# Optimization experiments

Measured on AMD Instinct MI355X. Metric: run time of the kernel, lower is better.

## Reference

```python
import jax, jax.numpy as jnp
import numpy as np

H, DM, DK, DV, DFF = 8, 512, 64, 64, 2048
B, S = 8, 1024
EPS = 1e-5


def layernorm_global(x):
    # torch nn.LayerNorm(x.size()[1:], elementwise_affine=False): normalize over ALL dims except batch
    mu = jnp.mean(x, axis=(1, 2), keepdims=True)
    var = jnp.var(x, axis=(1, 2), keepdims=True)
    return (x - mu) / jnp.sqrt(var + EPS)


def mha(q_in, k_in, v_in, wq, bq, wk, bk, wv, bv, wo, bo, causal):
    # wq/wk: [h, dk, dmodel], wv: [h, dv, dmodel] (torch Linear weight layout [out,in])
    q = jnp.einsum('bsd,hkd->bhsk', q_in, wq) + bq[None, :, None, :]
    k = jnp.einsum('bsd,hkd->bhsk', k_in, wk) + bk[None, :, None, :]
    v = jnp.einsum('bsd,hvd->bhsv', v_in, wv) + bv[None, :, None, :]
    scores = jnp.einsum('bhqk,bhsk->bhqs', q, k) / np.sqrt(DK).astype(np.float32)
    if causal:
        Sq = q_in.shape[1]
        mask = jnp.triu(jnp.full((Sq, Sq), -jnp.inf, dtype=scores.dtype), k=1)
        scores = scores + mask[None, None, :, :]
    w = jax.nn.softmax(scores, axis=-1)
    attn = jnp.einsum('bhqs,bhsv->bhqv', w, v)  # [b,h,q,dv]
    concat = attn.transpose(0, 2, 1, 3).reshape(q_in.shape[0], q_in.shape[1], H * DV)
    return concat @ wo.T + bo


def setup_inputs() -> dict:
    key = jax.random.key(0)
    ks = jax.random.split(key, 24)
    f = lambda k, shape: (jax.random.normal(k, shape, dtype=jnp.float32) * 0.02)
    inp = {
        'x_enc': jax.random.normal(ks[0], (B, S, DM), dtype=jnp.float32),
        'x_dec': jax.random.normal(ks[1], (B, S, DM), dtype=jnp.float32),
        # masked self-attention params
        'mq_w': f(ks[2], (H, DK, DM)), 'mq_b': f(ks[3], (H, DK)),
        'mk_w': f(ks[4], (H, DK, DM)), 'mk_b': f(ks[5], (H, DK)),
        'mv_w': f(ks[6], (H, DV, DM)), 'mv_b': f(ks[7], (H, DV)),
        'mo_w': f(ks[8], (DM, H * DV)), 'mo_b': f(ks[9], (DM,)),
        # cross-attention params
        'cq_w': f(ks[10], (H, DK, DM)), 'cq_b': f(ks[11], (H, DK)),
        'ck_w': f(ks[12], (H, DK, DM)), 'ck_b': f(ks[13], (H, DK)),
        'cv_w': f(ks[14], (H, DV, DM)), 'cv_b': f(ks[15], (H, DV)),
        'co_w': f(ks[16], (DM, H * DV)), 'co_b': f(ks[17], (DM,)),
        # feedforward params
        'f1_w': f(ks[18], (DFF, DM)), 'f1_b': f(ks[19], (DFF,)),
        'f2_w': f(ks[20], (DM, DFF)), 'f2_b': f(ks[21], (DM,)),
    }
    return inp


def reference(x_enc, x_dec,
              mq_w, mq_b, mk_w, mk_b, mv_w, mv_b, mo_w, mo_b,
              cq_w, cq_b, ck_w, ck_b, cv_w, cv_b, co_w, co_b,
              f1_w, f1_b, f2_w, f2_b):
    # masked self-attention block (dropout = identity at eval)
    x_dec_n = layernorm_global(x_dec)
    sa = mha(x_dec_n, x_dec_n, x_dec_n, mq_w, mq_b, mk_w, mk_b, mv_w, mv_b, mo_w, mo_b, causal=True)
    current = x_dec + sa
    # cross-attention block
    cur_n = layernorm_global(current)
    enc_n = layernorm_global(x_enc)
    ca = mha(cur_n, enc_n, enc_n, cq_w, cq_b, ck_w, ck_b, cv_w, cv_b, co_w, co_b, causal=False)
    result = current + ca
    # feedforward block
    res_n = layernorm_global(result)
    ff = jax.nn.relu(res_n @ f1_w.T + f1_b) @ f2_w.T + f2_b
    return result + ff
```

## Files before the change

### kernel.cpp

```cpp
#include <hip/hip_runtime.h>
#include <cmath>
#include <cstddef>
#include <cstdint>

#define BN   8
#define SN   1024
#define DMN  512
#define HN   8
#define DKN  64
#define DFFN 2048

typedef short           bf16x8   __attribute__((ext_vector_type(8)));
typedef float           f32x4    __attribute__((ext_vector_type(4)));
typedef float           f32x16   __attribute__((ext_vector_type(16)));
typedef unsigned short  ushortx4 __attribute__((ext_vector_type(4)));
typedef unsigned short  ushortx8 __attribute__((ext_vector_type(8)));
typedef unsigned int    uintx4   __attribute__((ext_vector_type(4)));
typedef unsigned short  u16;
typedef unsigned int    u32;

__device__ __forceinline__ float bf2f(u16 u) {
  return __uint_as_float(((unsigned int)u) << 16);
}
__device__ __forceinline__ u16 f2bf(float f) {
  unsigned int u = __float_as_uint(f);
  u += 0x7FFFu + ((u >> 16) & 1u);
  return (u16)(u >> 16);
}
__device__ __forceinline__ u32 cvtpk_bf16(float lo, float hi) {
  u32 r;
  asm("v_cvt_pk_bf16_f32 %0, %1, %2" : "=v"(r) : "v"(lo), "v"(hi));
  return r;
}
__device__ __forceinline__ void gload_lds16(const u16* gsrc, u16* ldst) {
  __builtin_amdgcn_global_load_lds(
      (const __attribute__((address_space(1))) unsigned int*)gsrc,
      (__attribute__((address_space(3))) unsigned int*)ldst,
      16, 0, 0);
}

__global__ __launch_bounds__(256) void cvt_weights(
    const float* p0, const float* p1, const float* p2, const float* p3,
    const float* p4, const float* p5, const float* p6, const float* p7,
    const float* p8, const float* p9, u16* __restrict__ dst) {
  const int gi = blockIdx.x * 256 + threadIdx.x;
  const int idx = gi * 4;
  const float* src; int off;
  if (idx < 2097152) {
    const int t = idx >> 18; off = idx & 262143;
    switch (t) {
      case 0: src = p0; break; case 1: src = p1; break;
      case 2: src = p2; break; case 3: src = p3; break;
      case 4: src = p4; break; case 5: src = p5; break;
      case 6: src = p6; break; default: src = p7; break;
    }
  } else if (idx < 3145728) { src = p8; off = idx - 2097152; }
  else                      { src = p9; off = idx - 3145728; }
  float4 v = *(const float4*)(src + off);
  ushortx4 o;
  o[0] = f2bf(v.x); o[1] = f2bf(v.y); o[2] = f2bf(v.z); o[3] = f2bf(v.w);
  *(ushortx4*)(dst + idx) = o;
}

__global__ __launch_bounds__(256) void pack_bias(const float* a, const float* b,
                                                 const float* c, const float* d,
                                                 const float* e, float* __restrict__ dst) {
  const int t = threadIdx.x;
#pragma unroll
  for (int i = t; i < 512; i += 256) {
    dst[i]        = a[i];
    dst[512 + i]  = b[i];
    dst[1024 + i] = c[i];
    dst[1536 + i] = d[i];
    dst[2048 + i] = e[i];
  }
}

__global__ __launch_bounds__(256) void ln_sum(const float* __restrict__ X,
                                              float2* __restrict__ part) {
  const int g = blockIdx.x, b = blockIdx.y, t = threadIdx.x;
  const float4* Xv = (const float4*)(X + (size_t)b * (SN * DMN) + (size_t)g * 8192);
  float s = 0.f, s2 = 0.f;
#pragma unroll
  for (int it = 0; it < 8; ++it) {
    float4 x = Xv[t + it * 256];
    s  += x.x + x.y + x.z + x.w;
    s2 += x.x*x.x + x.y*x.y + x.z*x.z + x.w*x.w;
  }
  __shared__ float rs[256], rq[256];
  rs[t] = s; rq[t] = s2;
  __syncthreads();
  for (int off = 128; off > 0; off >>= 1) {
    if (t < off) { rs[t] += rs[t + off]; rq[t] += rq[t + off]; }
    __syncthreads();
  }
  if (t == 0) part[b * 64 + g] = make_float2(rs[0], rq[0]);
}

__global__ __launch_bounds__(256) void ln_norm(const float* __restrict__ X,
                                               const float2* __restrict__ part,
                                               u16* __restrict__ Y) {
  const int g = blockIdx.x, b = blockIdx.y, t = threadIdx.x;
  __shared__ float ss[64], sq[64];
  if (t < 64) { float2 p = part[b * 64 + t]; ss[t] = p.x; sq[t] = p.y; }
  __syncthreads();
  float s = 0.f, q = 0.f;
#pragma unroll
  for (int j = 0; j < 64; ++j) { s += ss[j]; q += sq[j]; }
  const float inv_n = 1.f / (float)(SN * DMN);
  const float mu = s * inv_n;
  const float var = q * inv_n - mu * mu;
  const float rstd = rsqrtf(var + 1e-5f);
  const size_t base = (size_t)b * (SN * DMN) + (size_t)g * 8192;
  const float4* Xv = (const float4*)(X + base);
#pragma unroll
  for (int it = 0; it < 8; ++it) {
    float4 x = Xv[t + it * 256];
    ushortx4 o;
    o[0] = f2bf((x.x - mu) * rstd); o[1] = f2bf((x.y - mu) * rstd);
    o[2] = f2bf((x.z - mu) * rstd); o[3] = f2bf((x.w - mu) * rstd);
    *(ushortx4*)(Y + base + (size_t)(t + it * 256) * 4) = o;
  }
}

template<bool RELU, bool RES, int OMODE, int BM>
__global__ __launch_bounds__(256) void gemm_mfma(const u16* __restrict__ A,
                                                 const u16* __restrict__ W,
                                                 const float* __restrict__ bias,
                                                 const float* __restrict__ res,
                                                 void* __restrict__ Cv,
                                                 void* __restrict__ Cv2,
                                                 void* __restrict__ Cv3,
                                                 int M, int N, int K) {
  constexpr int MI = BM / 32;
  __shared__ u16 As[BM * 32];
  __shared__ u16 Bs[128 * 32];
  const int t = threadIdx.x;
  const int lane = t & 63, w = t >> 6;
  const int wm = w >> 1, wn = w & 1;
  const int m0 = blockIdx.y * BM, n0 = blockIdx.x * 128;

  f32x4 acc[MI][4];
#pragma unroll
  for (int i = 0; i < MI; ++i)
#pragma unroll
    for (int j = 0; j < 4; ++j)
      acc[i][j] = (f32x4){0.f, 0.f, 0.f, 0.f};

  const int lrow = lane >> 2;
  const int lcol = (lane & 3) * 8;
  const int rofs = (lane & 15) * 32 + (lane >> 4) * 8;

  for (int k0 = 0; k0 < K; k0 += 32) {
    if (BM == 128) {
#pragma unroll
      for (int c = 0; c < 2; ++c) {
        const int r0 = w * 32 + c * 16;
        gload_lds16(A + (size_t)(m0 + r0 + lrow) * K + k0 + lcol, &As[r0 * 32]);
      }
    } else {
      const int r0 = w * 16;
      gload_lds16(A + (size_t)(m0 + r0 + lrow) * K + k0 + lcol, &As[r0 * 32]);
    }
#pragma unroll
    for (int c = 0; c < 2; ++c) {
      const int r0 = w * 32 + c * 16;
      gload_lds16(W + (size_t)(n0 + r0 + lrow) * K + k0 + lcol, &Bs[r0 * 32]);
    }
    __syncthreads();
    bf16x8 af[MI], bfr[4];
#pragma unroll
    for (int f = 0; f < MI; ++f)
      af[f]  = *(const bf16x8*)&As[(wm * (BM / 2) + f * 16) * 32 + rofs];
#pragma unroll
    for (int f = 0; f < 4; ++f)
      bfr[f] = *(const bf16x8*)&Bs[(wn * 64 + f * 16) * 32 + rofs];
#pragma unroll
    for (int i = 0; i < MI; ++i)
#pragma unroll
      for (int j = 0; j < 4; ++j)
        acc[i][j] = __builtin_amdgcn_mfma_f32_16x16x32_bf16(af[i], bfr[j], acc[i][j], 0, 0, 0);
    __syncthreads();
  }

  const int crow0 = (lane >> 4) * 4;
  const int ccol  = lane & 15;
  float bv[4];
#pragma unroll
  for (int j = 0; j < 4; ++j) bv[j] = bias[n0 + wn * 64 + j * 16 + ccol];

  u16* seg_out = nullptr;
  int  seg_n0 = 0;
  bool seg_vt = false;
  if (OMODE == 3) {
    if (n0 < 512)       { seg_out = (u16*)Cv;  seg_n0 = 0; }
    else if (n0 < 1024) { seg_out = (u16*)Cv2; seg_n0 = 512; }
    else                { seg_out = (u16*)Cv3; seg_n0 = 1024; seg_vt = true; }
  } else if (OMODE == 4) {
    if (n0 < 512)       { seg_out = (u16*)Cv;  seg_n0 = 0; }
    else                { seg_out = (u16*)Cv3; seg_n0 = 512; seg_vt = true; }
  }

#pragma unroll
  for (int i = 0; i < MI; ++i) {
#pragma unroll
    for (int r = 0; r < 4; ++r) {
      const int m = m0 + wm * (BM / 2) + i * 16 + crow0 + r;
#pragma unroll
      for (int j = 0; j < 4; ++j) {
        const int n = n0 + wn * 64 + j * 16 + ccol;
        float v = acc[i][j][r] + bv[j];
        if (RELU) v = fmaxf(v, 0.f);
        if (RES)  v += res[(size_t)m * N + n];
        if (OMODE == 0) {
          ((float*)Cv)[(size_t)m * N + n] = v;
        } else if (OMODE == 1) {
          ((u16*)Cv)[(size_t)m * N + n] = f2bf(v);
        } else {
          const int nn = n - seg_n0;
          if (!seg_vt) seg_out[(size_t)m * 512 + nn] = f2bf(v);
          else
            seg_out[(((size_t)(m >> 10) * HN + (nn >> 6)) * 64 + (nn & 63)) * SN + (m & 1023)] = f2bf(v);
        }
      }
    }
  }
}

#define QBLK 128
#define KVB  64

template<int CAUSAL>
__global__ __launch_bounds__(256) void attn_mfma(const u16* __restrict__ Q,
                                                 const u16* __restrict__ K,
                                                 const u16* __restrict__ VT,
                                                 u16* __restrict__ O) {
  const int qb = blockIdx.x;
  const int bh = blockIdx.y;
  const int b = bh >> 3, h = bh & 7;
  const int t = threadIdx.x;
  const int lane = t & 63, w = t >> 6;
  const int l31 = lane & 31, hi = lane >> 5;

  __shared__ __align__(16) u16 Ks[64 * 64];
  __shared__ __align__(16) u16 Vts[8 * 512];

  const int qw0 = qb * QBLK + w * 32;
  const int qglob = qw0 + l31;

  bf16x8 bq[4];
#pragma unroll
  for (int dk = 0; dk < 4; ++dk)
    bq[dk] = *(const bf16x8*)(Q + (size_t)(b * SN + qglob) * 512
                                + h * 64 + dk * 16 + hi * 8);

  f32x16 acc0 = {}, acc1 = {};
  float m_run = -INFINITY, l_run = 0.f;

  const int srow = t >> 2;
  const int ss0  = 2 * (t & 3);
  const u16* kg0 = K + (size_t)(b * SN + srow) * 512 + h * 64 + ((ss0 ^ (srow & 7)) * 8);
  const u16* kg1 = K + (size_t)(b * SN + srow) * 512 + h * 64 + (((ss0 + 1) ^ (srow & 7)) * 8);
  u16* kd0 = &Ks[t * 16];
  u16* kd1 = &Ks[t * 16 + 8];
  const int vd = t & 63, vp = t >> 6;
  const u16* vg = VT + ((size_t)bh * 64 + vd) * SN + vp * 16;
  u16* vdst0 = &Vts[(2 * vp) * 512 + vd * 8];
  u16* vdst1 = &Vts[(2 * vp + 1) * 512 + vd * 8];

  ushortx8 kr0, kr1, vr0, vr1;
  kr0 = *(const ushortx8*)kg0;
  kr1 = *(const ushortx8*)kg1;
  vr0 = *(const ushortx8*)vg;
  vr1 = *(const ushortx8*)(vg + 8);

  const int nkt = CAUSAL ? (2 * qb + 2) : (SN / KVB);
  for (int kt = 0; kt < nkt; ++kt) {
    const int k0 = kt * KVB;
    __syncthreads();
    *(ushortx8*)kd0 = kr0;
    *(ushortx8*)kd1 = kr1;
    *(ushortx8*)vdst0 = vr0;
    *(ushortx8*)vdst1 = vr1;
    if (kt + 1 < nkt) {
      const size_t kadv = (size_t)(kt + 1) * KVB * 512;
      kr0 = *(const ushortx8*)(kg0 + kadv);
      kr1 = *(const ushortx8*)(kg1 + kadv);
      vr0 = *(const ushortx8*)(vg + (kt + 1) * KVB);
      vr1 = *(const ushortx8*)(vg + (kt + 1) * KVB + 8);
    }
    __syncthreads();

    if (CAUSAL && k0 > qw0 + 31) continue;

    f32x16 s0 = {}, s1 = {};
#pragma unroll
    for (int dk = 0; dk < 4; ++dk) {
      const int boff = dk * 32 + hi * 16;
      const int sw = boff ^ ((l31 & 7) << 4);
      bf16x8 a0 = *(const bf16x8*)&Ks[l31 * 64 + (sw >> 1)];
      bf16x8 a1 = *(const bf16x8*)&Ks[(32 + l31) * 64 + (sw >> 1)];
      s0 = __builtin_amdgcn_mfma_f32_32x32x16_bf16(a0, bq[dk], s0, 0, 0, 0);
      s1 = __builtin_amdgcn_mfma_f32_32x32x16_bf16(a1, bq[dk], s1, 0, 0, 0);
    }

    const bool domask = CAUSAL && (k0 + KVB - 1 > qw0);
    float mx = -INFINITY;
#pragma unroll
    for (int i = 0; i < 16; ++i) {
      const int krow = (i & 3) + 8 * (i >> 2) + 4 * hi;
      float v0 = s0[i] * 0.125f;
      float v1 = s1[i] * 0.125f;
      if (domask) {
        if (k0 + krow > qglob)      v0 = -INFINITY;
        if (k0 + 32 + krow > qglob) v1 = -INFINITY;
      }
      s0[i] = v0; s1[i] = v1;
      mx = fmaxf(mx, fmaxf(v0, v1));
    }
    mx = fmaxf(mx, __shfl_xor(mx, 32));
    const float mn = fmaxf(m_run, mx);
    const float al = __expf(m_run - mn);
    m_run = mn;
    float ps = 0.f;
#pragma unroll
    for (int i = 0; i < 16; ++i) {
      s0[i] = __expf(s0[i] - mn); ps += s0[i];
      s1[i] = __expf(s1[i] - mn); ps += s1[i];
    }
    ps += __shfl_xor(ps, 32);
    l_run = l_run * al + ps;
    acc0 *= al;
    acc1 *= al;

#pragma unroll
    for (int ksb = 0; ksb < 4; ++ksb) {
      const int kb = ksb & 1;
      u32 A0, A1, B0, B1;
      if (ksb < 2) {
        A0 = cvtpk_bf16(s0[8*kb + 0], s0[8*kb + 1]);
        A1 = cvtpk_bf16(s0[8*kb + 2], s0[8*kb + 3]);
        B0 = cvtpk_bf16(s0[8*kb + 4], s0[8*kb + 5]);
        B1 = cvtpk_bf16(s0[8*kb + 6], s0[8*kb + 7]);
      } else {
        A0 = cvtpk_bf16(s1[8*kb + 0], s1[8*kb + 1]);
        A1 = cvtpk_bf16(s1[8*kb + 2], s1[8*kb + 3]);
        B0 = cvtpk_bf16(s1[8*kb + 4], s1[8*kb + 5]);
        B1 = cvtpk_bf16(s1[8*kb + 6], s1[8*kb + 7]);
      }
      const u32 xA0 = __shfl_xor(A0, 32), xA1 = __shfl_xor(A1, 32);
      const u32 xB0 = __shfl_xor(B0, 32), xB1 = __shfl_xor(B1, 32);
      uintx4 pw;
      pw[0] = hi ? xB0 : A0;
      pw[1] = hi ? xB1 : A1;
      pw[2] = hi ? B0 : xA0;
      pw[3] = hi ? B1 : xA1;
      const bf16x8 pb = *(const bf16x8*)&pw;
      const bf16x8 av0 = *(const bf16x8*)&Vts[(ksb * 2 + hi) * 512 + l31 * 8];
      const bf16x8 av1 = *(const bf16x8*)&Vts[(ksb * 2 + hi) * 512 + (32 + l31) * 8];
      acc0 = __builtin_amdgcn_mfma_f32_32x32x16_bf16(av0, pb, acc0, 0, 0, 0);
      acc1 = __builtin_amdgcn_mfma_f32_32x32x16_bf16(av1, pb, acc1, 0, 0, 0);
    }
  }

  const float inv = 1.f / l_run;
  u16* op = O + (size_t)(b * SN + qglob) * 512 + h * 64;
#pragma unroll
  for (int g = 0; g < 4; ++g) {
    ushortx4 o0, o1;
#pragma unroll
    for (int r = 0; r < 4; ++r) {
      o0[r] = f2bf(acc0[4*g + r] * inv);
      o1[r] = f2bf(acc1[4*g + r] * inv);
    }
    *(ushortx4*)(op + 4*hi + 8*g)      = o0;
    *(ushortx4*)(op + 32 + 4*hi + 8*g) = o1;
  }
}

extern "C" void kernel_launch(void* const* d_in, const int* in_sizes, int n_in,
                              void* d_out, int out_size, void* d_ws, size_t ws_size,
                              hipStream_t stream) {
  const float* x_enc = (const float*)d_in[0];
  const float* x_dec = (const float*)d_in[1];
  const float* mq_w = (const float*)d_in[2];  const float* mq_b = (const float*)d_in[3];
  const float* mk_w = (const float*)d_in[4];  const float* mk_b = (const float*)d_in[5];
  const float* mv_w = (const float*)d_in[6];  const float* mv_b = (const float*)d_in[7];
  const float* mo_w = (const float*)d_in[8];  const float* mo_b = (const float*)d_in[9];
  const float* cq_w = (const float*)d_in[10]; const float* cq_b = (const float*)d_in[11];
  const float* ck_w = (const float*)d_in[12]; const float* ck_b = (const float*)d_in[13];
  const float* cv_w = (const float*)d_in[14]; const float* cv_b = (const float*)d_in[15];
  const float* co_w = (const float*)d_in[16]; const float* co_b = (const float*)d_in[17];
  const float* f1_w = (const float*)d_in[18]; const float* f1_b = (const float*)d_in[19];
  const float* f2_w = (const float*)d_in[20]; const float* f2_b = (const float*)d_in[21];
  float* out = (float*)d_out;

  char* wsb = (char*)d_ws;
  float* o5  = (float*)(wsb + 0);
  float* o6  = (float*)(wsb + (16u << 20));
  u16* Qb    = (u16*)(wsb + (32u << 20));
  u16* Kb    = (u16*)(wsb + (40u << 20));
  u16* VTb   = (u16*)(wsb + (48u << 20));
  u16* B0    = (u16*)(wsb + (56u << 20));
  u16* B1    = (u16*)(wsb + (64u << 20));
  u16* FF1   = (u16*)(wsb + (72u << 20));
  u16* WB    = (u16*)(wsb + (104u << 20));
  float2* part = (float2*)(wsb + (112u << 20));
  float* BC  = (float*)(wsb + (113u << 20));

  u16* wb_mq = WB + 0 * 262144;
  u16* wb_mo = WB + 3 * 262144;
  u16* wb_cq = WB + 4 * 262144;
  u16* wb_ck = WB + 5 * 262144;
  u16* wb_co = WB + 7 * 262144;
  u16* wb_f1 = WB + 8 * 262144; u16* wb_f2 = WB + 8 * 262144 + 1048576;

  const int M = BN * SN;
  dim3 ln_grid(64, BN);
  dim3 g512s(512 / 128, M / 64);
  dim3 g1024(1024 / 128, M / 128);
  dim3 g1536(1536 / 128, M / 128);
  dim3 g2048(2048 / 128, M / 128);
  dim3 attn_grid(SN / QBLK, BN * HN);

  cvt_weights<<<4096, 256, 0, stream>>>(mq_w, mk_w, mv_w, mo_w, cq_w, ck_w, cv_w, co_w,
                                        f1_w, f2_w, WB);
  pack_bias<<<1, 256, 0, stream>>>(mq_b, mk_b, mv_b, ck_b, cv_b, BC);

  ln_sum<<<ln_grid, 256, 0, stream>>>(x_dec, part);
  ln_norm<<<ln_grid, 256, 0, stream>>>(x_dec, part, B0);
  gemm_mfma<false, false, 3, 128><<<g1536, 256, 0, stream>>>(B0, wb_mq, BC, nullptr,
                                                             Qb, Kb, VTb, M, 1536, 512);
  attn_mfma<1><<<attn_grid, 256, 0, stream>>>(Qb, Kb, VTb, B0);
  gemm_mfma<false, true, 0, 64><<<g512s, 256, 0, stream>>>(B0, wb_mo, mo_b, x_dec,
                                                           o5, nullptr, nullptr, M, 512, 512);

  ln_sum<<<ln_grid, 256, 0, stream>>>(o5, part);
  ln_norm<<<ln_grid, 256, 0, stream>>>(o5, part, B0);
  ln_sum<<<ln_grid, 256, 0, stream>>>(x_enc, part);
  ln_norm<<<ln_grid, 256, 0, stream>>>(x_enc, part, B1);
  gemm_mfma<false, false, 1, 64><<<g512s, 256, 0, stream>>>(B0, wb_cq, cq_b, nullptr,
                                                            Qb, nullptr, nullptr, M, 512, 512);
  gemm_mfma<false, false, 4, 128><<<g1024, 256, 0, stream>>>(B1, wb_ck, BC + 1536, nullptr,
                                                             Kb, nullptr, VTb, M, 1024, 512);
  attn_mfma<0><<<attn_grid, 256, 0, stream>>>(Qb, Kb, VTb, B0);
  gemm_mfma<false, true, 0, 64><<<g512s, 256, 0, stream>>>(B0, wb_co, co_b, o5,
                                                           o6, nullptr, nullptr, M, 512, 512);

  ln_sum<<<ln_grid, 256, 0, stream>>>(o6, part);
  ln_norm<<<ln_grid, 256, 0, stream>>>(o6, part, B0);
  gemm_mfma<true, false, 1, 128><<<g2048, 256, 0, stream>>>(B0, wb_f1, f1_b, nullptr,
                                                            FF1, nullptr, nullptr, M, 2048, 512);
  gemm_mfma<false, true, 0, 64><<<g512s, 256, 0, stream>>>(FF1, wb_f2, f2_b, o6,
                                                           out, nullptr, nullptr, M, 512, 2048);
}
```

Baseline: 300.1 us.

## Split attention KV range four ways with merge kernel; fold softmax scale into Q

Attention now runs with a third grid dimension that splits the key/value tiles into four chunks. Each chunk writes its unnormalized partial output plus its running max and sum. A new merge kernel combines the four chunks with log-sum-exp weights and normalizes the result. Separately, the 1/sqrt(dk)*log2(e) factor is folded into the Q projection epilogue so the softmax can use exp2 without a per-score multiply. The aim is to raise block count and reduce causal load imbalance, at the cost of extra partial-result traffic and one more launch per attention.

```diff
diff --git a/kernel.cpp b/kernel.cpp
--- a/kernel.cpp
+++ b/kernel.cpp
@@ -18,6 +18,8 @@
 typedef unsigned int    uintx4   __attribute__((ext_vector_type(4)));
 typedef unsigned short  u16;
 typedef unsigned int    u32;
+
+#define ATT_SC 0.18033688011112042f
 
 __device__ __forceinline__ float bf2f(u16 u) {
   return __uint_as_float(((unsigned int)u) << 16);
@@ -123,7 +125,7 @@
   }
 }
 
-template<bool RELU, bool RES, int OMODE, int BM>
+template<bool RELU, bool RES, int OMODE, int BM, bool QSC>
 __global__ __launch_bounds__(256) void gemm_mfma(const u16* __restrict__ A,
                                                  const u16* __restrict__ W,
                                                  const float* __restrict__ bias,
@@ -200,6 +202,7 @@
     if (n0 < 512)       { seg_out = (u16*)Cv;  seg_n0 = 0; }
     else                { seg_out = (u16*)Cv3; seg_n0 = 512; seg_vt = true; }
   }
+  const bool do_scale = QSC && (OMODE != 3 || n0 < 512);
 
 #pragma unroll
   for (int i = 0; i < MI; ++i) {
@@ -212,6 +215,7 @@
         float v = acc[i][j][r] + bv[j];
         if (RELU) v = fmaxf(v, 0.f);
         if (RES)  v += res[(size_t)m * N + n];
+        if (do_scale) v *= ATT_SC;
         if (OMODE == 0) {
           ((float*)Cv)[(size_t)m * N + n] = v;
         } else if (OMODE == 1) {
@@ -230,13 +234,15 @@
 #define QBLK 128
 #define KVB  64
 
-template<int CAUSAL>
+template<int CAUSAL, int NSPLIT>
 __global__ __launch_bounds__(256) void attn_mfma(const u16* __restrict__ Q,
                                                  const u16* __restrict__ K,
                                                  const u16* __restrict__ VT,
-                                                 u16* __restrict__ O) {
+                                                 u16* __restrict__ Pacc,
+                                                 float2* __restrict__ ML) {
   const int qb = blockIdx.x;
   const int bh = blockIdx.y;
+  const int sp = blockIdx.z;
   const int b = bh >> 3, h = bh & 7;
   const int t = threadIdx.x;
   const int lane = t & 63, w = t >> 6;
@@ -256,6 +262,11 @@
 
   f32x16 acc0 = {}, acc1 = {};
   float m_run = -INFINITY, l_run = 0.f;
+
+  const int ntile = CAUSAL ? (2 * qb + 2) : (SN / KVB);
+  const int n4 = (ntile + NSPLIT - 1) / NSPLIT;
+  const int kt0 = sp * n4;
+  const int ktend = (kt0 + n4 < ntile) ? (kt0 + n4) : ntile;
 
   const int srow = t >> 2;
   const int ss0  = 2 * (t & 3);
@@ -269,20 +280,22 @@
   u16* vdst1 = &Vts[(2 * vp + 1) * 512 + vd * 8];
 
   ushortx8 kr0, kr1, vr0, vr1;
-  kr0 = *(const ushortx8*)kg0;
-  kr1 = *(const ushortx8*)kg1;
-  vr0 = *(const ushortx8*)vg;
-  vr1 = *(const ushortx8*)(vg + 8);
-
-  const int nkt = CAUSAL ? (2 * qb + 2) : (SN / KVB);
-  for (int kt = 0; kt < nkt; ++kt) {
+  {
+    const size_t ka = (size_t)kt0 * KVB * 512;
+    kr0 = *(const ushortx8*)(kg0 + ka);
+    kr1 = *(const ushortx8*)(kg1 + ka);
+    vr0 = *(const ushortx8*)(vg + kt0 * KVB);
+    vr1 = *(const ushortx8*)(vg + kt0 * KVB + 8);
+  }
+
+  for (int kt = kt0; kt < ktend; ++kt) {
     const int k0 = kt * KVB;
     __syncthreads();
     *(ushortx8*)kd0 = kr0;
     *(ushortx8*)kd1 = kr1;
     *(ushortx8*)vdst0 = vr0;
     *(ushortx8*)vdst1 = vr1;
-    if (kt + 1 < nkt) {
+    if (kt + 1 < ktend) {
       const size_t kadv = (size_t)(kt + 1) * KVB * 512;
       kr0 = *(const ushortx8*)(kg0 + kadv);
       kr1 = *(const ushortx8*)(kg1 + kadv);
@@ -309,8 +322,8 @@
 #pragma unroll
     for (int i = 0; i < 16; ++i) {
       const int krow = (i & 3) + 8 * (i >> 2) + 4 * hi;
-      float v0 = s0[i] * 0.125f;
-      float v1 = s1[i] * 0.125f;
+      float v0 = s0[i];
+      float v1 = s1[i];
       if (domask) {
         if (k0 + krow > qglob)      v0 = -INFINITY;
         if (k0 + 32 + krow > qglob) v1 = -INFINITY;
@@ -320,13 +333,13 @@
     }
     mx = fmaxf(mx, __shfl_xor(mx, 32));
     const float mn = fmaxf(m_run, mx);
-    const float al = __expf(m_run - mn);
+    const float al = exp2f(m_run - mn);
     m_run = mn;
     float ps = 0.f;
 #pragma unroll
     for (int i = 0; i < 16; ++i) {
-      s0[i] = __expf(s0[i] - mn); ps += s0[i];
-      s1[i] = __expf(s1[i] - mn); ps += s1[i];
+      s0[i] = exp2f(s0[i] - mn); ps += s0[i];
+      s1[i] = exp2f(s1[i] - mn); ps += s1[i];
     }
     ps += __shfl_xor(ps, 32);
     l_run = l_run * al + ps;
@@ -363,19 +376,59 @@
     }
   }
 
-  const float inv = 1.f / l_run;
-  u16* op = O + (size_t)(b * SN + qglob) * 512 + h * 64;
+  u16* op = Pacc + (((size_t)(sp * 64 + bh)) * 1024 + qglob) * 64;
 #pragma unroll
   for (int g = 0; g < 4; ++g) {
     ushortx4 o0, o1;
 #pragma unroll
     for (int r = 0; r < 4; ++r) {
-      o0[r] = f2bf(acc0[4*g + r] * inv);
-      o1[r] = f2bf(acc1[4*g + r] * inv);
+      o0[r] = f2bf(acc0[4*g + r]);
+      o1[r] = f2bf(acc1[4*g + r]);
     }
     *(ushortx4*)(op + 4*hi + 8*g)      = o0;
     *(ushortx4*)(op + 32 + 4*hi + 8*g) = o1;
   }
+  if (hi == 0)
+    ML[((size_t)(sp * 64 + bh)) * 1024 + qglob] = make_float2(m_run, l_run);
+}
+
+__global__ __launch_bounds__(256) void attn_merge(const u16* __restrict__ Pacc,
+                                                  const float2* __restrict__ ML,
+                                                  u16* __restrict__ O) {
+  const int tid = blockIdx.x * 256 + threadIdx.x;
+  const int qh = tid >> 3;
+  const int d0 = (tid & 7) * 8;
+  const int b = qh >> 13, q = (qh >> 3) & 1023, h = qh & 7;
+  const int bh = b * 8 + h;
+
+  float m2[4], ls[4];
+  float M2 = -INFINITY;
+#pragma unroll
+  for (int s = 0; s < 4; ++s) {
+    float2 p = ML[((size_t)(s * 64 + bh)) * 1024 + q];
+    m2[s] = p.x; ls[s] = p.y;
+    M2 = fmaxf(M2, m2[s]);
+  }
+  float lt = 0.f, wgt[4];
+#pragma unroll
+  for (int s = 0; s < 4; ++s) {
+    wgt[s] = (ls[s] > 0.f) ? exp2f(m2[s] - M2) : 0.f;
+    lt += ls[s] * wgt[s];
+  }
+  const float inv = 1.f / lt;
+  float o[8] = {};
+#pragma unroll
+  for (int s = 0; s < 4; ++s) {
+    if (wgt[s] > 0.f) {
+      ushortx8 a = *(const ushortx8*)(Pacc + (((size_t)(s * 64 + bh)) * 1024 + q) * 64 + d0);
+#pragma unroll
+      for (int e = 0; e < 8; ++e) o[e] += wgt[s] * bf2f(a[e]);
+    }
+  }
+  ushortx8 ov;
+#pragma unroll
+  for (int e = 0; e < 8; ++e) ov[e] = f2bf(o[e] * inv);
+  *(ushortx8*)(O + ((size_t)(b * 1024 + q) * 512) + h * 64 + d0) = ov;
 }
 
 extern "C" void kernel_launch(void* const* d_in, const int* in_sizes, int n_in,
@@ -408,6 +461,9 @@
   float2* part = (float2*)(wsb + (112u << 20));
   float* BC  = (float*)(wsb + (113u << 20));
 
+  u16* Pacc   = FF1;
+  float2* ML  = (float2*)B1;
+
   u16* wb_mq = WB + 0 * 262144;
   u16* wb_mo = WB + 3 * 262144;
   u16* wb_cq = WB + 4 * 262144;
@@ -421,7 +477,7 @@
   dim3 g1024(1024 / 128, M / 128);
   dim3 g1536(1536 / 128, M / 128);
   dim3 g2048(2048 / 128, M / 128);
-  dim3 attn_grid(SN / QBLK, BN * HN);
+  dim3 attn_grid(SN / QBLK, BN * HN, 4);
 
   cvt_weights<<<4096, 256, 0, stream>>>(mq_w, mk_w, mv_w, mo_w, cq_w, ck_w, cv_w, co_w,
                                         f1_w, f2_w, WB);
@@ -429,28 +485,30 @@
 
   ln_sum<<<ln_grid, 256, 0, stream>>>(x_dec, part);
   ln_norm<<<ln_grid, 256, 0, stream>>>(x_dec, part, B0);
-  gemm_mfma<false, false, 3, 128><<<g1536, 256, 0, stream>>>(B0, wb_mq, BC, nullptr,
-                                                             Qb, Kb, VTb, M, 1536, 512);
-  attn_mfma<1><<<attn_grid, 256, 0, stream>>>(Qb, Kb, VTb, B0);
-  gemm_mfma<false, true, 0, 64><<<g512s, 256, 0, stream>>>(B0, wb_mo, mo_b, x_dec,
-                                                           o5, nullptr, nullptr, M, 512, 512);
+  gemm_mfma<false, false, 3, 128, true><<<g1536, 256, 0, stream>>>(B0, wb_mq, BC, nullptr,
+                                                                   Qb, Kb, VTb, M, 1536, 512);
+  attn_mfma<1, 4><<<attn_grid, 256, 0, stream>>>(Qb, Kb, VTb, Pacc, ML);
+  attn_merge<<<2048, 256, 0, stream>>>(Pacc, ML, B0);
+  gemm_mfma<false, true, 0, 64, false><<<g512s, 256, 0, stream>>>(B0, wb_mo, mo_b, x_dec,
+                                                                  o5, nullptr, nullptr, M, 512, 512);
 
   ln_sum<<<ln_grid, 256, 0, stream>>>(o5, part);
   ln_norm<<<ln_grid, 256, 0, stream>>>(o5, part, B0);
   ln_sum<<<ln_grid, 256, 0, stream>>>(x_enc, part);
   ln_norm<<<ln_grid, 256, 0, stream>>>(x_enc, part, B1);
-  gemm_mfma<false, false, 1, 64><<<g512s, 256, 0, stream>>>(B0, wb_cq, cq_b, nullptr,
-                                                            Qb, nullptr, nullptr, M, 512, 512);
-  gemm_mfma<false, false, 4, 128><<<g1024, 256, 0, stream>>>(B1, wb_ck, BC + 1536, nullptr,
-                                                             Kb, nullptr, VTb, M, 1024, 512);
-  attn_mfma<0><<<attn_grid, 256, 0, stream>>>(Qb, Kb, VTb, B0);
-  gemm_mfma<false, true, 0, 64><<<g512s, 256, 0, stream>>>(B0, wb_co, co_b, o5,
-                                                           o6, nullptr, nullptr, M, 512, 512);
+  gemm_mfma<false, false, 1, 64, true><<<g512s, 256, 0, stream>>>(B0, wb_cq, cq_b, nullptr,
+                                                                  Qb, nullptr, nullptr, M, 512, 512);
+  gemm_mfma<false, false, 4, 128, false><<<g1024, 256, 0, stream>>>(B1, wb_ck, BC + 1536, nullptr,
+                                                                    Kb, nullptr, VTb, M, 1024, 512);
+  attn_mfma<0, 4><<<attn_grid, 256, 0, stream>>>(Qb, Kb, VTb, Pacc, ML);
+  attn_merge<<<2048, 256, 0, stream>>>(Pacc, ML, B0);
+  gemm_mfma<false, true, 0, 64, false><<<g512s, 256, 0, stream>>>(B0, wb_co, co_b, o5,
+                                                                  o6, nullptr, nullptr, M, 512, 512);
 
   ln_sum<<<ln_grid, 256, 0, stream>>>(o6, part);
   ln_norm<<<ln_grid, 256, 0, stream>>>(o6, part, B0);
-  gemm_mfma<true, false, 1, 128><<<g2048, 256, 0, stream>>>(B0, wb_f1, f1_b, nullptr,
-                                                            FF1, nullptr, nullptr, M, 2048, 512);
-  gemm_mfma<false, true, 0, 64><<<g512s, 256, 0, stream>>>(FF1, wb_f2, f2_b, o6,
-                                                           out, nullptr, nullptr, M, 512, 2048);
-}
+  gemm_mfma<true, false, 1, 128, false><<<g2048, 256, 0, stream>>>(B0, wb_f1, f1_b, nullptr,
+                                                                   FF1, nullptr, nullptr, M, 2048, 512);
+  gemm_mfma<false, true, 0, 64, false><<<g512s, 256, 0, stream>>>(FF1, wb_f2, f2_b, o6,
+                                                                  out, nullptr, nullptr, M, 512, 2048);
+}
```

Measured after the change: 322.7 us. +7.5%, slower.
